# Performance work log

Measured on AMD Instinct MI355X. Metric: run time of the kernel, lower is better.

The kernel has to match this reference:

```python
import jax, jax.numpy as jnp
import numpy as np

N = 50000  # nodes
E = 1600000  # edges
L = 2  # layers
D = 128  # input/hidden dim


def setup_inputs() -> dict:
    key = jax.random.key(0)
    ks = jax.random.split(key, 8)
    s = 1.0 / np.sqrt(D)
    return {
        "x": jax.random.normal(ks[0], (N, D), jnp.float32),
        "edge_index": jax.random.randint(ks[1], (2, E), 0, N, jnp.int64),
        "h": jax.random.normal(ks[2], (L, N, D), jnp.float32),
        "Wx": jax.random.normal(ks[3], (L, 3, D, D), jnp.float32) * s,
        "bx": jax.random.normal(ks[4], (L, 3, D), jnp.float32) * 0.01,
        "Wh": jax.random.normal(ks[5], (L, 3, D, D), jnp.float32) * s,
        "bh": jax.random.normal(ks[6], (L, 3, D), jnp.float32) * 0.01,
    }


def _gcn(x, W, b, src, dst, dinv):
    # GCNConv with added self-loops and symmetric normalization:
    # out = D^{-1/2} (A + I) D^{-1/2} X W + b
    hw = x @ W                                   # [N, H]
    norm = dinv[src] * dinv[dst]                 # [E]
    msg = hw[src] * norm[:, None]                # [E, H]
    agg = jax.ops.segment_sum(msg, dst, num_segments=N)
    agg = agg + hw * (dinv * dinv)[:, None]      # self-loop contribution
    return agg + b


def reference(x, edge_index, h, Wx, bx, Wh, bh):
    src = edge_index[0]
    dst = edge_index[1]
    # in-degree on destination nodes, including self-loop (+1)
    deg = jax.ops.segment_sum(jnp.ones((E,), x.dtype), dst, num_segments=N) + 1.0
    dinv = jax.lax.rsqrt(deg)

    outs = []
    inp = x
    for l in range(L):
        hl = h[l]
        z = jax.nn.sigmoid(_gcn(inp, Wx[l, 0], bx[l, 0], src, dst, dinv)
                           + _gcn(hl, Wh[l, 0], bh[l, 0], src, dst, dinv))
        r = jax.nn.sigmoid(_gcn(inp, Wx[l, 1], bx[l, 1], src, dst, dinv)
                           + _gcn(hl, Wh[l, 1], bh[l, 1], src, dst, dinv))
        h_tilde = jnp.tanh(_gcn(inp, Wx[l, 2], bx[l, 2], src, dst, dinv)
                           + _gcn(r * hl, Wh[l, 2], bh[l, 2], src, dst, dinv))
        out = z * hl + (1.0 - z) * h_tilde
        outs.append(out)
        inp = out
    return jnp.stack(outs, axis=0)  # [L, N, H]
```

## Files before the change

### kernel.cpp

```cpp
#include <hip/hip_runtime.h>

typedef __attribute__((ext_vector_type(8))) unsigned short us8;
typedef __attribute__((ext_vector_type(8))) short s8;
typedef __attribute__((ext_vector_type(4))) float f4;
typedef __attribute__((ext_vector_type(2))) float f2;

#define DEV static __device__ __forceinline__
#define CAP 128
#define NRG 128
#define NBB 256
#define SEGC 128

DEV float bf2f(unsigned short h){ return __uint_as_float(((unsigned)h)<<16); }
DEV unsigned short f2bf(float f){
  unsigned x = __float_as_uint(f);
  x += 0x7fffu + ((x>>16)&1u);
  return (unsigned short)(x>>16);
}
DEV float sigm(float x){ return 1.f/(1.f + __expf(-x)); }

__global__ __launch_bounds__(256) void k_bucket(const int* __restrict__ src,
    const int* __restrict__ dst, unsigned* __restrict__ buf,
    int* __restrict__ cnt2, int e, int n){
  __shared__ int lcnt[NRG];
  int b = blockIdx.x;
  for(int i=threadIdx.x;i<NRG;i+=256) lcnt[i] = 0;
  __syncthreads();
  int chunk = (e + NBB - 1)/NBB;
  int lo = b*chunk;
  int hi = lo + chunk; if(hi>e) hi=e;
  for(int i = lo + threadIdx.x; i < hi; i += 256){
    int d = dst[i], s = src[i];
    int r = (d*NRG)/n;
    int pos = atomicAdd(&lcnt[r], 1);
    if(pos < SEGC)
      buf[((size_t)r*NBB + b)*SEGC + pos] = ((unsigned)d<<16) | (unsigned)s;
  }
  __syncthreads();
  for(int i=threadIdx.x;i<NRG;i+=256) cnt2[i*NBB + b] = lcnt[i];
}

__global__ __launch_bounds__(256) void k_build2(const unsigned* __restrict__ buf,
    const int* __restrict__ cnt2, int* __restrict__ cnt,
    unsigned short* __restrict__ col, int n){
  int r = blockIdx.x;
  int lo = (r*n + NRG-1)/NRG;
  int hi = ((r+1)*n + NRG-1)/NRG;
  int span = hi - lo;
  __shared__ int lc[512];
  for(int i=threadIdx.x; i<span; i+=256) lc[i] = 0;
  __syncthreads();
  int lane = threadIdx.x & 63;
  for(int seg = threadIdx.x>>6; seg < NBB; seg += 4){
    int c = cnt2[r*NBB + seg]; if(c > SEGC) c = SEGC;
    const unsigned* p = buf + ((size_t)r*NBB + seg)*SEGC;
    for(int i = lane; i < c; i += 64){
      unsigned v = p[i];
      int d = (int)(v >> 16), s = (int)(v & 0xffffu);
      int slot = atomicAdd(&lc[d - lo], 1);
      col[(size_t)d*CAP + slot] = (unsigned short)s;
    }
  }
  __syncthreads();
  for(int i=threadIdx.x; i<span; i+=256) cnt[lo + i] = lc[i];
}

__global__ void k_setup(const int* __restrict__ cnt, float* __restrict__ dinv, int n,
                        const float* __restrict__ Wx, const float* __restrict__ Wh,
                        unsigned short* __restrict__ WT){
  int gN = (n + 255)/256;
  int b = blockIdx.x;
  if(b < gN){
    int i = b*256 + threadIdx.x;
    if(i<n) dinv[i] = rsqrtf((float)cnt[i] + 1.0f);
  } else {
    int i = (b-gN)*256 + threadIdx.x;
    int m = i >> 15;
    int rem = i & 32767;
    int j = rem >> 8;
    int k = rem & 255;
    float v = (k<128) ? Wx[((size_t)m*128 + k)*128 + j]
                      : Wh[((size_t)m*128 + (k-128))*128 + j];
    WT[(size_t)m*32768 + j*256 + k] = f2bf(v);
  }
}

__global__ void k_scale2(const float* __restrict__ inp, const float* __restrict__ hl,
                         const float* __restrict__ dinv, unsigned char* __restrict__ y2, int n){
  int i = blockIdx.x*blockDim.x+threadIdx.x;
  if(i >= n*32) return;
  int node = i>>5, d0 = (i&31)*4;
  float dv = dinv[node];
  f4 a = *(const f4*)(inp + (size_t)node*128 + d0);
  f4 b = *(const f4*)(hl  + (size_t)node*128 + d0);
  unsigned pa = __builtin_amdgcn_cvt_pk_fp8_f32(dv*a[0], dv*a[1], 0, false);
  pa = __builtin_amdgcn_cvt_pk_fp8_f32(dv*a[2], dv*a[3], pa, true);
  unsigned pb = __builtin_amdgcn_cvt_pk_fp8_f32(dv*b[0], dv*b[1], 0, false);
  pb = __builtin_amdgcn_cvt_pk_fp8_f32(dv*b[2], dv*b[3], pb, true);
  *(unsigned*)(y2 + (size_t)node*256 + d0)       = pa;
  *(unsigned*)(y2 + (size_t)node*256 + 128 + d0) = pb;
}

template<int DB>
__global__ __launch_bounds__(256) void k_agg(const unsigned char* __restrict__ y,
    const int* __restrict__ cnt, const unsigned short* __restrict__ col,
    const float* __restrict__ dinv, unsigned short* __restrict__ out0, int n)
{
  constexpr int GL = DB/16;
  constexpr int NG = 64/GL;
  constexpr int U = 8;
  int tid = threadIdx.x;
  int wave = tid>>6, lane = tid&63;
  int g = lane/GL, gl = lane%GL;
  int node = blockIdx.x*(4*NG) + wave*NG + g;
  if(node >= n) return;
  const unsigned char* yb = y + (size_t)gl*16;
  float acc[16];
  {
    uint4 q = *(const uint4*)(yb + (size_t)node*DB);
    const unsigned* qw = (const unsigned*)&q;
    #pragma unroll
    for(int w=0;w<4;++w){
      f2 lo = __builtin_amdgcn_cvt_pk_f32_fp8(qw[w], false);
      f2 hi = __builtin_amdgcn_cvt_pk_f32_fp8(qw[w], true);
      acc[w*4+0]=lo[0]; acc[w*4+1]=lo[1]; acc[w*4+2]=hi[0]; acc[w*4+3]=hi[1];
    }
  }
  const unsigned short* myrow = col + (size_t)node*CAP;
  int c_ = cnt[node];
  int last = c_ - 1;
  for(int i=0; i<c_; i += U){
    int s[U];
    #pragma unroll
    for(int u=0;u<U;++u){
      int ii = i + u; ii = (ii < last) ? ii : last;
      s[u] = myrow[ii];
    }
    uint4 v[U];
    #pragma unroll
    for(int u=0;u<U;++u) v[u] = *(const uint4*)(yb + (size_t)s[u]*DB);
    #pragma unroll
    for(int u=0;u<U;++u){
      if(i + u < c_){
        const unsigned* qw = (const unsigned*)&v[u];
        #pragma unroll
        for(int w=0;w<4;++w){
          f2 lo = __builtin_amdgcn_cvt_pk_f32_fp8(qw[w], false);
          f2 hi = __builtin_amdgcn_cvt_pk_f32_fp8(qw[w], true);
          acc[w*4+0]+=lo[0]; acc[w*4+1]+=lo[1]; acc[w*4+2]+=hi[0]; acc[w*4+3]+=hi[1];
        }
      }
    }
  }
  float dv = dinv[node];
  us8 w0, w1;
  #pragma unroll
  for(int j=0;j<8;++j){ w0[j]=f2bf(acc[j]*dv); w1[j]=f2bf(acc[8+j]*dv); }
  int c = gl*16;
  *(us8*)(out0 + (size_t)node*DB + c)     = w0;
  *(us8*)(out0 + (size_t)node*DB + c + 8) = w1;
}

template<int KB>
DEV void stageB512(unsigned char* Bs, const unsigned short* Bsrc, int srcStride,
                   int srcOff, int t){
  constexpr int CPR = KB/8;
  #pragma unroll
  for(int i=0;i<128*CPR/512;++i){
    int c = t + i*512;
    int j = c / CPR, kc = c % CPR;
    us8 v = *(const us8*)(Bsrc + (size_t)j*srcStride + srcOff + kc*8);
    *(us8*)(Bs + ((j*(KB*2) + kc*16) ^ ((j&7)<<4))) = v;
  }
}
template<int KB>
DEV void mfmaK(const unsigned char* Bs, const unsigned short* A, int astride,
               int arow, int nrows, int lo, int hi, f4 (&acc)[8]){
  const unsigned short* Ap = A + (size_t)(arow < nrows ? arow : 0)*astride + hi*8;
  #pragma unroll
  for(int kk=0;kk<KB/32;++kk){
    s8 a = (arow<nrows) ? *(const s8*)(Ap + kk*32) : (s8)(short)0;
    #pragma unroll
    for(int n=0;n<8;++n){
      int j = n*16+lo;
      s8 b = *(const s8*)(Bs + ((j*(KB*2) + kk*64 + hi*16) ^ ((lo&7)<<4)));
      acc[n] = __builtin_amdgcn_mfma_f32_16x16x32_bf16(a, b, acc[n], 0,0,0);
    }
  }
}

__global__ __launch_bounds__(512) void k_gemmRH(
    const unsigned short* __restrict__ axah, const unsigned short* __restrict__ Wr,
    const unsigned short* __restrict__ Wh2, const float* __restrict__ hl,
    const float* __restrict__ dinv, const float* __restrict__ bxr,
    const float* __restrict__ bhr, unsigned char* __restrict__ yq,
    unsigned short* __restrict__ Zbh, int nrows)
{
  __shared__ unsigned char Bs[65536];
  const int t = threadIdx.x, lane = t & 63, lo = lane & 15, hi = lane >> 4;
  const int r0 = blockIdx.x*128 + (t>>6)*16;
  const int arow = r0 + lo;
  f4 acc[8];
  #pragma unroll
  for(int n=0;n<8;++n) acc[n]=(f4)0.f;
  stageB512<256>(Bs, Wr, 256, 0, t);
  __syncthreads();
  mfmaK<256>(Bs, axah, 256, arow, nrows, lo, hi, acc);
  #pragma unroll
  for(int n=0;n<8;++n){
    const int colv = n*16 + lo;
    float bz = bxr[colv] + bhr[colv];
    #pragma unroll
    for(int tt=0;tt<4;++tt){
      int row = r0 + hi*4 + tt;
      if(row < nrows){
        float r = sigm(acc[n][tt] + bz);
        float q = dinv[row] * r * hl[(size_t)row*128 + colv];
        unsigned pk = __builtin_amdgcn_cvt_pk_fp8_f32(q, q, 0, false);
        yq[(size_t)row*128 + colv] = (unsigned char)(pk & 0xff);
      }
    }
  }
  __syncthreads();
  stageB512<128>(Bs, Wh2, 256, 0, t);
  __syncthreads();
  #pragma unroll
  for(int n=0;n<8;++n) acc[n]=(f4)0.f;
  mfmaK<128>(Bs, axah, 256, arow, nrows, lo, hi, acc);
  #pragma unroll
  for(int n=0;n<8;++n){
    const int colv = n*16 + lo;
    #pragma unroll
    for(int tt=0;tt<4;++tt){
      int row = r0 + hi*4 + tt;
      if(row < nrows) Zbh[(size_t)row*128 + colv] = f2bf(acc[n][tt]);
    }
  }
}

__global__ __launch_bounds__(512) void k_gemmZF(
    const unsigned short* __restrict__ axah, const unsigned short* __restrict__ aq,
    const unsigned short* __restrict__ Wz, const unsigned short* __restrict__ Wh2,
    const unsigned short* __restrict__ Zbh, const float* __restrict__ hl,
    const float* __restrict__ hnext, const float* __restrict__ dinv,
    const float* __restrict__ bxz, const float* __restrict__ bhz,
    const float* __restrict__ bxh, const float* __restrict__ bhh,
    float* __restrict__ outp, unsigned char* __restrict__ y2out, int nrows)
{
  __shared__ unsigned char Bs[65536];
  const int t = threadIdx.x, lane = t & 63, lo = lane & 15, hi = lane >> 4;
  const int r0 = blockIdx.x*128 + (t>>6)*16;
  const int arow = r0 + lo;
  f4 accZ[8], accH[8];
  #pragma unroll
  for(int n=0;n<8;++n){ accZ[n]=(f4)0.f; accH[n]=(f4)0.f; }
  stageB512<256>(Bs, Wz, 256, 0, t);
  __syncthreads();
  mfmaK<256>(Bs, axah, 256, arow, nrows, lo, hi, accZ);
  __syncthreads();
  stageB512<128>(Bs, Wh2, 256, 128, t);
  __syncthreads();
  mfmaK<128>(Bs, aq, 128, arow, nrows, lo, hi, accH);
  #pragma unroll
  for(int n=0;n<8;++n){
    const int colv = n*16 + lo;
    float bz = bxz[colv] + bhz[colv];
    float bh = bxh[colv] + bhh[colv];
    #pragma unroll
    for(int tt=0;tt<4;++tt){
      int row = r0 + hi*4 + tt;
      if(row >= nrows) continue;
      float z  = sigm(accZ[n][tt] + bz);
      float ht = tanhf(accH[n][tt] + bf2f(Zbh[(size_t)row*128 + colv]) + bh);
      float ov = z*hl[(size_t)row*128 + colv] + (1.f - z)*ht;
      outp[(size_t)row*128 + colv] = ov;
      if(y2out){
        float dv = dinv[row];
        unsigned pk = __builtin_amdgcn_cvt_pk_fp8_f32(dv*ov, dv*ov, 0, false);
        y2out[(size_t)row*256 + colv] = (unsigned char)(pk & 0xff);
        float hv = dv * hnext[(size_t)row*128 + colv];
        unsigned ph = __builtin_amdgcn_cvt_pk_fp8_f32(hv, hv, 0, false);
        y2out[(size_t)row*256 + 128 + colv] = (unsigned char)(ph & 0xff);
      }
    }
  }
}

extern "C" void kernel_launch(void* const* d_in, const int* in_sizes, int n_in,
                              void* d_out, int out_size, void* d_ws, size_t ws_size,
                              hipStream_t stream){
  const float* x  = (const float*)d_in[0];
  const int*   ei = (const int*)d_in[1];
  const float* h  = (const float*)d_in[2];
  const float* Wx = (const float*)d_in[3];
  const float* bx = (const float*)d_in[4];
  const float* Wh = (const float*)d_in[5];
  const float* bh = (const float*)d_in[6];
  float* out = (float*)d_out;

  const int N = in_sizes[0] / 128;
  const int E = in_sizes[1] / 2;
  const int L = in_sizes[2] / in_sizes[0];
  const int* src = ei;
  const int* dst = ei + E;

  char* w = (char*)d_ws;
  auto alloc = [&](size_t b)->char*{ char* p = w; w += (b + 255) & ~(size_t)255; return p; };
  int* cnt = (int*)alloc((size_t)N*sizeof(int));
  unsigned short* col = (unsigned short*)alloc((size_t)N*CAP*sizeof(short));
  float* dinv = (float*)alloc((size_t)N*sizeof(float));
  unsigned short* WT = (unsigned short*)alloc((size_t)6*32768*sizeof(short));
  unsigned char* y2 = (unsigned char*)alloc((size_t)N*256);
  unsigned short* axah = (unsigned short*)alloc((size_t)N*256*sizeof(short));
  unsigned char* yq = (unsigned char*)alloc((size_t)N*128);
  unsigned short* aq = (unsigned short*)alloc((size_t)N*128*sizeof(short));
  unsigned short* Zbh = (unsigned short*)alloc((size_t)N*128*sizeof(short));
  unsigned* ebuf = (unsigned*)alloc((size_t)NRG*NBB*SEGC*sizeof(unsigned));
  int* cnt2 = (int*)alloc((size_t)NRG*NBB*sizeof(int));

  const int gN = (N + 255)/256;
  const int gew = (N*32 + 255)/256;
  const int g128 = (N + 127)/128;
  const int gagg4 = (N + 15)/16;
  const int gagg2 = (N + 31)/32;

  k_bucket<<<NBB,256,0,stream>>>(src, dst, ebuf, cnt2, E, N);
  k_build2<<<NRG,256,0,stream>>>(ebuf, cnt2, cnt, col, N);
  k_setup<<<gN + 768,256,0,stream>>>(cnt, dinv, N, Wx, Wh, WT);

  for(int l=0; l<L; ++l){
    const float* hl  = h + (size_t)l*N*128;
    const float* bxz = bx + (size_t)(l*3+0)*128; const float* bhz = bh + (size_t)(l*3+0)*128;
    const float* bxr = bx + (size_t)(l*3+1)*128; const float* bhr = bh + (size_t)(l*3+1)*128;
    const float* bxh = bx + (size_t)(l*3+2)*128; const float* bhh = bh + (size_t)(l*3+2)*128;
    const unsigned short* Wz = WT + (size_t)(l*3+0)*32768;
    const unsigned short* Wr = WT + (size_t)(l*3+1)*32768;
    const unsigned short* Wh2= WT + (size_t)(l*3+2)*32768;

    if(l==0) k_scale2<<<gew,256,0,stream>>>(x, hl, dinv, y2, N);
    k_agg<256><<<gagg4,256,0,stream>>>(y2, cnt, col, dinv, axah, N);
    k_gemmRH<<<g128,512,0,stream>>>(axah, Wr, Wh2, hl, dinv, bxr, bhr, yq, Zbh, N);
    k_agg<128><<<gagg2,256,0,stream>>>(yq, cnt, col, dinv, aq, N);
    k_gemmZF<<<g128,512,0,stream>>>(axah, aq, Wz, Wh2, Zbh, hl,
        (l+1<L) ? (h + (size_t)(l+1)*N*128) : nullptr, dinv,
        bxz, bhz, bxh, bhh, out + (size_t)l*N*128,
        (l+1<L) ? y2 : nullptr, N);
  }
}
```

Baseline: 382.1 us.

## Halve GEMM block size, split K staging into 128-wide chunks, reuse A registers

```diff
diff --git a/kernel.cpp b/kernel.cpp
--- a/kernel.cpp
+++ b/kernel.cpp
@@ -161,51 +161,64 @@
   *(us8*)(out0 + (size_t)node*DB + c + 8) = w1;
 }
 
-template<int KB>
-DEV void stageB512(unsigned char* Bs, const unsigned short* Bsrc, int srcStride,
-                   int srcOff, int t){
-  constexpr int CPR = KB/8;
-  #pragma unroll
-  for(int i=0;i<128*CPR/512;++i){
-    int c = t + i*512;
-    int j = c / CPR, kc = c % CPR;
-    us8 v = *(const us8*)(Bsrc + (size_t)j*srcStride + srcOff + kc*8);
-    *(us8*)(Bs + ((j*(KB*2) + kc*16) ^ ((j&7)<<4))) = v;
-  }
-}
-template<int KB>
-DEV void mfmaK(const unsigned char* Bs, const unsigned short* A, int astride,
-               int arow, int nrows, int lo, int hi, f4 (&acc)[8]){
-  const unsigned short* Ap = A + (size_t)(arow < nrows ? arow : 0)*astride + hi*8;
-  #pragma unroll
-  for(int kk=0;kk<KB/32;++kk){
-    s8 a = (arow<nrows) ? *(const s8*)(Ap + kk*32) : (s8)(short)0;
+DEV void stageB256(unsigned char* Bs, const unsigned short* Bsrc, int srcOff, int t){
+  #pragma unroll
+  for(int i=0;i<8;++i){
+    int c = t + i*256;
+    int j = c >> 4, kc = c & 15;
+    us8 v = *(const us8*)(Bsrc + (size_t)j*256 + srcOff + kc*8);
+    *(us8*)(Bs + ((j*256 + kc*16) ^ ((j&7)<<4))) = v;
+  }
+}
+DEV void loadA4(const unsigned short* A, int astride, int arow, int nrows, int hi,
+                int koff, s8 (&a)[4]){
+  const unsigned short* Ap = A + (size_t)(arow < nrows ? arow : 0)*astride + koff + hi*8;
+  #pragma unroll
+  for(int kk=0;kk<4;++kk) a[kk] = *(const s8*)(Ap + kk*32);
+  if(arow >= nrows){
+    #pragma unroll
+    for(int kk=0;kk<4;++kk) a[kk] = (s8)(short)0;
+  }
+}
+DEV void mfma128(const unsigned char* Bs, const s8 (&a)[4], int lo, int hi,
+                 f4 (&acc)[8]){
+  #pragma unroll
+  for(int kk=0;kk<4;++kk){
     #pragma unroll
     for(int n=0;n<8;++n){
       int j = n*16+lo;
-      s8 b = *(const s8*)(Bs + ((j*(KB*2) + kk*64 + hi*16) ^ ((lo&7)<<4)));
-      acc[n] = __builtin_amdgcn_mfma_f32_16x16x32_bf16(a, b, acc[n], 0,0,0);
-    }
-  }
-}
-
-__global__ __launch_bounds__(512) void k_gemmRH(
+      s8 b = *(const s8*)(Bs + ((j*256 + kk*64 + hi*16) ^ ((lo&7)<<4)));
+      acc[n] = __builtin_amdgcn_mfma_f32_16x16x32_bf16(a[kk], b, acc[n], 0,0,0);
+    }
+  }
+}
+
+__global__ __launch_bounds__(256) void k_gemmRH(
     const unsigned short* __restrict__ axah, const unsigned short* __restrict__ Wr,
     const unsigned short* __restrict__ Wh2, const float* __restrict__ hl,
     const float* __restrict__ dinv, const float* __restrict__ bxr,
     const float* __restrict__ bhr, unsigned char* __restrict__ yq,
     unsigned short* __restrict__ Zbh, int nrows)
 {
-  __shared__ unsigned char Bs[65536];
+  __shared__ unsigned char Bs[32768];
   const int t = threadIdx.x, lane = t & 63, lo = lane & 15, hi = lane >> 4;
-  const int r0 = blockIdx.x*128 + (t>>6)*16;
+  const int r0 = blockIdx.x*64 + (t>>6)*16;
   const int arow = r0 + lo;
-  f4 acc[8];
-  #pragma unroll
-  for(int n=0;n<8;++n) acc[n]=(f4)0.f;
-  stageB512<256>(Bs, Wr, 256, 0, t);
-  __syncthreads();
-  mfmaK<256>(Bs, axah, 256, arow, nrows, lo, hi, acc);
+  s8 a03[4], a47[4];
+  f4 accR[8], accH[8];
+  #pragma unroll
+  for(int n=0;n<8;++n){ accR[n]=(f4)0.f; accH[n]=(f4)0.f; }
+  loadA4(axah, 256, arow, nrows, hi, 0, a03);
+  stageB256(Bs, Wr, 0, t);
+  __syncthreads();
+  mfma128(Bs, a03, lo, hi, accR);
+  __syncthreads();
+  loadA4(axah, 256, arow, nrows, hi, 128, a47);
+  stageB256(Bs, Wr, 128, t);
+  __syncthreads();
+  mfma128(Bs, a47, lo, hi, accR);
+  __syncthreads();
+  stageB256(Bs, Wh2, 0, t);
   #pragma unroll
   for(int n=0;n<8;++n){
     const int colv = n*16 + lo;
@@ -214,7 +227,7 @@
     for(int tt=0;tt<4;++tt){
       int row = r0 + hi*4 + tt;
       if(row < nrows){
-        float r = sigm(acc[n][tt] + bz);
+        float r = sigm(accR[n][tt] + bz);
         float q = dinv[row] * r * hl[(size_t)row*128 + colv];
         unsigned pk = __builtin_amdgcn_cvt_pk_fp8_f32(q, q, 0, false);
         yq[(size_t)row*128 + colv] = (unsigned char)(pk & 0xff);
@@ -222,23 +235,19 @@
     }
   }
   __syncthreads();
-  stageB512<128>(Bs, Wh2, 256, 0, t);
-  __syncthreads();
-  #pragma unroll
-  for(int n=0;n<8;++n) acc[n]=(f4)0.f;
-  mfmaK<128>(Bs, axah, 256, arow, nrows, lo, hi, acc);
+  mfma128(Bs, a03, lo, hi, accH);
   #pragma unroll
   for(int n=0;n<8;++n){
     const int colv = n*16 + lo;
     #pragma unroll
     for(int tt=0;tt<4;++tt){
       int row = r0 + hi*4 + tt;
-      if(row < nrows) Zbh[(size_t)row*128 + colv] = f2bf(acc[n][tt]);
-    }
-  }
-}
-
-__global__ __launch_bounds__(512) void k_gemmZF(
+      if(row < nrows) Zbh[(size_t)row*128 + colv] = f2bf(accH[n][tt]);
+    }
+  }
+}
+
+__global__ __launch_bounds__(256) void k_gemmZF(
     const unsigned short* __restrict__ axah, const unsigned short* __restrict__ aq,
     const unsigned short* __restrict__ Wz, const unsigned short* __restrict__ Wh2,
     const unsigned short* __restrict__ Zbh, const float* __restrict__ hl,
@@ -247,20 +256,28 @@
     const float* __restrict__ bxh, const float* __restrict__ bhh,
     float* __restrict__ outp, unsigned char* __restrict__ y2out, int nrows)
 {
-  __shared__ unsigned char Bs[65536];
+  __shared__ unsigned char Bs[32768];
   const int t = threadIdx.x, lane = t & 63, lo = lane & 15, hi = lane >> 4;
-  const int r0 = blockIdx.x*128 + (t>>6)*16;
+  const int r0 = blockIdx.x*64 + (t>>6)*16;
   const int arow = r0 + lo;
+  s8 a[4];
   f4 accZ[8], accH[8];
   #pragma unroll
   for(int n=0;n<8;++n){ accZ[n]=(f4)0.f; accH[n]=(f4)0.f; }
-  stageB512<256>(Bs, Wz, 256, 0, t);
-  __syncthreads();
-  mfmaK<256>(Bs, axah, 256, arow, nrows, lo, hi, accZ);
-  __syncthreads();
-  stageB512<128>(Bs, Wh2, 256, 128, t);
-  __syncthreads();
-  mfmaK<128>(Bs, aq, 128, arow, nrows, lo, hi, accH);
+  loadA4(axah, 256, arow, nrows, hi, 0, a);
+  stageB256(Bs, Wz, 0, t);
+  __syncthreads();
+  mfma128(Bs, a, lo, hi, accZ);
+  __syncthreads();
+  loadA4(axah, 256, arow, nrows, hi, 128, a);
+  stageB256(Bs, Wz, 128, t);
+  __syncthreads();
+  mfma128(Bs, a, lo, hi, accZ);
+  __syncthreads();
+  loadA4(aq, 128, arow, nrows, hi, 0, a);
+  stageB256(Bs, Wh2, 128, t);
+  __syncthreads();
+  mfma128(Bs, a, lo, hi, accH);
   #pragma unroll
   for(int n=0;n<8;++n){
     const int colv = n*16 + lo;
@@ -320,7 +337,7 @@
 
   const int gN = (N + 255)/256;
   const int gew = (N*32 + 255)/256;
-  const int g128 = (N + 127)/128;
+  const int g64 = (N + 63)/64;
   const int gagg4 = (N + 15)/16;
   const int gagg2 = (N + 31)/32;
 
@@ -339,9 +356,9 @@
 
     if(l==0) k_scale2<<<gew,256,0,stream>>>(x, hl, dinv, y2, N);
     k_agg<256><<<gagg4,256,0,stream>>>(y2, cnt, col, dinv, axah, N);
-    k_gemmRH<<<g128,512,0,stream>>>(axah, Wr, Wh2, hl, dinv, bxr, bhr, yq, Zbh, N);
+    k_gemmRH<<<g64,256,0,stream>>>(axah, Wr, Wh2, hl, dinv, bxr, bhr, yq, Zbh, N);
     k_agg<128><<<gagg2,256,0,stream>>>(yq, cnt, col, dinv, aq, N);
-    k_gemmZF<<<g128,512,0,stream>>>(axah, aq, Wz, Wh2, Zbh, hl,
+    k_gemmZF<<<g64,256,0,stream>>>(axah, aq, Wz, Wh2, Zbh, hl,
         (l+1<L) ? (h + (size_t)(l+1)*N*128) : nullptr, dinv,
         bxz, bhz, bxh, bhh, out + (size_t)l*N*128,
         (l+1<L) ? y2 : nullptr, N);
```

New measurement: 428.3 us. +12.1%, slower.
